# Kernel tuning notes

Hardware: AMD Instinct MI355X
Metric: run time of the kernel (lower is better)

The kernel has to match this reference:

```python
import math
import jax, jax.numpy as jnp
import numpy as np

B, L, D = 32, 512, 768
PAD, SEP = 0, 102
NEG = -9e15


def setup_inputs() -> dict:
    key = jax.random.key(0)
    ks = jax.random.split(key, 24)
    x = jax.random.normal(ks[0], (B, L, D), jnp.float32)
    # token ids: real tokens in [103, 30000), one SEP mid-sequence, PAD tail
    tok = jax.random.randint(ks[1], (B, L), 103, 30000)
    valid_len = jax.random.randint(ks[2], (B,), L // 2, L + 1)
    sep_pos = valid_len // 2
    pos = jnp.arange(L)[None, :]
    x_ids = jnp.where(pos < valid_len[:, None], tok, PAD)
    x_ids = jnp.where(pos == sep_pos[:, None], SEP, x_ids)

    s = 0.02
    def w(k, shape):
        return jax.random.normal(k, shape, jnp.float32) * s

    inp = dict(x=x, x_ids=x_ids, pad_idx=PAD, sep_idx=SEP)
    inp['W_anom'] = w(ks[3], (D, 1)); inp['b_anom'] = jnp.zeros((1,), jnp.float32)
    names = ['Wq_sup', 'Wk_sup', 'Wq_con', 'Wk_con', 'Wq_rep', 'Wk_rep']
    for i, n in enumerate(names):
        inp[n] = w(ks[4 + i], (D, D))
        inp[n.replace('W', 'b')] = jnp.zeros((D,), jnp.float32)
    inp['W_fuse1'] = w(ks[10], (3 * D, D)); inp['b_fuse1'] = jnp.zeros((D,), jnp.float32)
    inp['W_fuse2'] = w(ks[11], (D, D)); inp['b_fuse2'] = jnp.zeros((D,), jnp.float32)
    inp['ln_g'] = jnp.ones((D,), jnp.float32); inp['ln_b'] = jnp.zeros((D,), jnp.float32)
    return inp


def _segment_masks(x_ids, pad_idx, sep_idx, L):
    sep_mask = x_ids == sep_idx
    has_sep = sep_mask.any(axis=1)
    idxs = jnp.argmax(sep_mask.astype(jnp.int32), axis=1)
    valid_mask = x_ids != pad_idx
    valid_len = valid_mask.sum(axis=1)
    fallback = jnp.clip(valid_len // 2, 1, max(1, L - 2))
    sep_pos = jnp.where(has_sep, idxs, fallback)
    pos = jnp.arange(L)[None, :]
    false_mask = (pos < sep_pos[:, None]) & valid_mask
    option_mask = (pos > sep_pos[:, None]) & valid_mask
    return false_mask, option_mask


def reference(x, x_ids, pad_idx, sep_idx,
              W_anom, b_anom,
              Wq_sup, bq_sup, Wk_sup, bk_sup,
              Wq_con, bq_con, Wk_con, bk_con,
              Wq_rep, bq_rep, Wk_rep, bk_rep,
              W_fuse1, b_fuse1, W_fuse2, b_fuse2,
              ln_g, ln_b):
    Bx, Lx, Dm = x.shape
    false_mask, option_mask = _segment_masks(x_ids, pad_idx, sep_idx, Lx)

    # anomaly gate over the false (pre-SEP) segment
    anom = (x @ W_anom)[..., 0] + b_anom[0]                      # [B,L]
    anom = jnp.where(false_mask, anom, NEG)
    gate = jax.nn.softmax(anom, axis=1) * false_mask
    gate = gate / jnp.clip(gate.sum(axis=1, keepdims=True), 1e-8)

    inv = 1.0 / math.sqrt(Dm)
    q_sup = x @ Wq_sup + bq_sup; k_sup = x @ Wk_sup + bk_sup
    q_con = x @ Wq_con + bq_con; k_con = x @ Wk_con + bk_con
    q_rep = x @ Wq_rep + bq_rep; k_rep = x @ Wk_rep + bk_rep

    sup_scores = jnp.einsum('bld,bmd->blm', q_sup, k_sup) * inv   # [B,L,L]
    con_scores = jnp.einsum('bld,bmd->blm', q_con, k_con) * inv
    rep_scores = jnp.einsum('bld,bmd->blm', q_rep, k_rep) * inv

    pair_mask = false_mask[:, :, None] & option_mask[:, None, :]  # [B,L,L]
    sup_attn = jax.nn.softmax(jnp.where(pair_mask, sup_scores, NEG), axis=-1)
    conflict_signed = jnp.tanh(con_scores)
    rep_attn = jax.nn.softmax(jnp.where(pair_mask, rep_scores + conflict_signed, NEG), axis=-1)

    repair_token_vec = jnp.einsum('blm,bmd->bld', rep_attn, x)
    support_token_vec = jnp.einsum('blm,bmd->bld', sup_attn, x)

    anomaly_false_vec = jnp.einsum('bl,bld->bd', gate, x)
    weighted_repair_vec = jnp.einsum('bl,bld->bd', gate, repair_token_vec)
    weighted_support_vec = jnp.einsum('bl,bld->bd', gate, support_token_vec)

    fused = jnp.concatenate([anomaly_false_vec, weighted_repair_vec, weighted_support_vec], axis=-1)
    fused = jax.nn.relu(fused @ W_fuse1 + b_fuse1) @ W_fuse2 + b_fuse2  # dropout = identity (eval)

    mu = fused.mean(axis=-1, keepdims=True)
    var = ((fused - mu) ** 2).mean(axis=-1, keepdims=True)
    fused = (fused - mu) / jnp.sqrt(var + 1e-5) * ln_g + ln_b
    return fused
```

## Files before the change

kernel.cpp:

```cpp
#include <hip/hip_runtime.h>
#include <hip/hip_bf16.h>

#define B_ 32
#define L_ 512
#define D_ 768
#define M_ (B_*L_)
#define NEGV (-9e15f)

typedef __hip_bfloat16 bf16;
typedef short v8s __attribute__((ext_vector_type(8)));
typedef float v4f __attribute__((ext_vector_type(4)));

static __device__ __forceinline__ unsigned short f2b(float f) {
    __hip_bfloat16 h = __float2bfloat16(f);
    return *reinterpret_cast<unsigned short*>(&h);
}

static __device__ __forceinline__ float fast_tanh(float x) {
    x = fminf(fmaxf(x, -15.f), 15.f);
    float e2 = __expf(2.f * x);
    return (e2 - 1.f) / (e2 + 1.f);
}

static __device__ __forceinline__ void gl_lds16(const void* g, void* l) {
    __builtin_amdgcn_global_load_lds(
        (const __attribute__((address_space(1))) unsigned int*)g,
        (__attribute__((address_space(3))) unsigned int*)l, 16, 0, 0);
}

static __device__ __forceinline__ v8s pack8(const float* p) {
    v8s r;
    #pragma unroll
    for (int i = 0; i < 8; i++) r[i] = (short)f2b(p[i]);
    return r;
}

__global__ __launch_bounds__(256) void k_setup(const int* ids, const int* pad_p, const int* sep_p, int* seg,
                        const float* Wk_sup, const float* bq_sup,
                        const float* Wk_con, const float* bq_con,
                        const float* Wk_rep, const float* bq_rep,
                        const float* Wq_con, const float* bk_con,
                        float* __restrict__ vecs) {
    int bid = blockIdx.x, t = threadIdx.x;
    if (bid < 32) {
        int b = bid;
        __shared__ int red[256];
        int pad = *pad_p, sepid = *sep_p;
        int minsep = L_, vcount = 0;
        for (int l = t; l < L_; l += 256) {
            int id = ids[b*L_ + l];
            if (id == sepid && l < minsep) minsep = l;
            if (id != pad) vcount++;
        }
        red[t] = minsep; __syncthreads();
        for (int s = 128; s > 0; s >>= 1) { if (t < s) red[t] = min(red[t], red[t+s]); __syncthreads(); }
        int sepmin = red[0]; __syncthreads();
        red[t] = vcount; __syncthreads();
        for (int s = 128; s > 0; s >>= 1) { if (t < s) red[t] += red[t+s]; __syncthreads(); }
        if (t == 0) {
            int vlen = red[0];
            int fb = vlen / 2; if (fb < 1) fb = 1; if (fb > L_-2) fb = L_-2;
            int sep = (sepmin < L_) ? sepmin : fb;
            seg[b*2] = sep; seg[b*2+1] = vlen;
        }
        return;
    }
    {
        int gw = (bid - 32)*4 + (t >> 6);
        int lane = t & 63;
        if (gw > 3072) return;
        if (gw == 3072) {
            float s = 0.f;
            #pragma unroll
            for (int i = 0; i < D_/64; i++) s += bq_con[lane + 64*i] * bk_con[lane + 64*i];
            #pragma unroll
            for (int m = 32; m; m >>= 1) s += __shfl_xor(s, m);
            if (lane == 0) vecs[3072] = s;
            return;
        }
        int sel = gw / D_, row = gw % D_;
        const float* Wrow; const float* bv;
        switch (sel) {
            case 0: Wrow = Wk_sup + (size_t)row*D_; bv = bq_sup; break;
            case 1: Wrow = Wk_con + (size_t)row*D_; bv = bq_con; break;
            case 2: Wrow = Wk_rep + (size_t)row*D_; bv = bq_rep; break;
            default: Wrow = Wq_con + (size_t)row*D_; bv = bk_con; break;
        }
        float s = 0.f;
        #pragma unroll
        for (int i = 0; i < D_/64; i++) s += Wrow[lane + 64*i] * bv[lane + 64*i];
        #pragma unroll
        for (int m = 32; m; m >>= 1) s += __shfl_xor(s, m);
        if (lane == 0) vecs[gw] = s;
    }
}

__global__ void k_prep(const float* __restrict__ x, const float* __restrict__ Wa,
                       const float* __restrict__ ba, const float* __restrict__ vecs,
                       bf16* __restrict__ xb,
                       float* __restrict__ anom, float* __restrict__ csup,
                       float* __restrict__ ccon, float* __restrict__ crep,
                       float* __restrict__ rcon) {
    int gw = (blockIdx.x*blockDim.x + threadIdx.x) >> 6;
    int lane = threadIdx.x & 63;
    if (gw >= M_) return;
    const float* xr = x + (size_t)gw*D_;
    bf16* xbr = xb + (size_t)gw*D_;
    float sa=0.f, s0=0.f, s1=0.f, s2=0.f, s3=0.f;
    #pragma unroll
    for (int i = 0; i < D_/64; i++) {
        int o = i*64 + lane;
        float xv = xr[o];
        xbr[o] = __float2bfloat16(xv);
        sa += xv * Wa[o];
        s0 += xv * vecs[o];
        s1 += xv * vecs[768 + o];
        s2 += xv * vecs[1536 + o];
        s3 += xv * vecs[2304 + o];
    }
    #pragma unroll
    for (int m = 32; m; m >>= 1) {
        sa += __shfl_xor(sa, m); s0 += __shfl_xor(s0, m); s1 += __shfl_xor(s1, m);
        s2 += __shfl_xor(s2, m); s3 += __shfl_xor(s3, m);
    }
    if (lane == 0) {
        anom[gw] = sa + ba[0];
        csup[gw] = s0; ccon[gw] = s1; crep[gw] = s2; rcon[gw] = s3;
    }
}

__global__ void k_gate(const float* __restrict__ anom, const int* __restrict__ ids,
                       const int* seg, const int* pad_p, float* __restrict__ gate,
                       float4* __restrict__ zbuf, int zcount4) {
    int b = blockIdx.x, t = threadIdx.x;
    for (int i = b*256 + t; i < zcount4; i += 32*256)
        zbuf[i] = (float4){0.f,0.f,0.f,0.f};
    int sep = seg[b*2]; int pad = *pad_p;
    __shared__ float red[256];
    float a0[2]; bool f0[2];
    float mx = -__builtin_inff();
    #pragma unroll
    for (int j = 0; j < 2; j++) {
        int l = t + j*256;
        bool fm = (l < sep) && (ids[b*L_+l] != pad);
        float a = anom[b*L_+l];
        f0[j] = fm; a0[j] = a;
        if (fm) mx = fmaxf(mx, a);
    }
    red[t] = mx; __syncthreads();
    for (int s = 128; s; s >>= 1) { if (t < s) red[t] = fmaxf(red[t], red[t+s]); __syncthreads(); }
    mx = red[0]; __syncthreads();
    float e[2]; float se = 0.f;
    #pragma unroll
    for (int j = 0; j < 2; j++) { e[j] = f0[j] ? __expf(a0[j]-mx) : 0.f; se += e[j]; }
    red[t] = se; __syncthreads();
    for (int s = 128; s; s >>= 1) { if (t < s) red[t] += red[t+s]; __syncthreads(); }
    se = red[0];
    float inv = 1.f / fmaxf(se, 1e-8f);
    #pragma unroll
    for (int j = 0; j < 2; j++) { int l = t + j*256; gate[b*L_+l] = e[j]*inv; }
}

__global__ __launch_bounds__(256) void k_wqk(const float* Wq_sup, const float* Wk_sup,
                                             const float* Wq_con, const float* Wk_con,
                                             const float* Wq_rep, const float* Wk_rep,
                                             bf16* __restrict__ AT) {
    int h = blockIdx.z;
    const float* Asrc; const float* Bsrc;
    switch (h) { case 0: Asrc=Wk_sup; Bsrc=Wq_sup; break;
                 case 1: Asrc=Wk_con; Bsrc=Wq_con; break;
                 default: Asrc=Wk_rep; Bsrc=Wq_rep; }
    bf16* outp = AT + (size_t)h*D_*D_;
    __shared__ bf16 As[64*32];
    __shared__ bf16 Bs[64*32];
    int t = threadIdx.x;
    int wave = t >> 6, lane = t & 63;
    int quad = lane >> 4, l16 = lane & 15;
    int wm = wave >> 1, wn = wave & 1;
    int row0 = blockIdx.x * 64;
    int col0 = blockIdx.y * 64;

    v4f acc[2][2];
    #pragma unroll
    for (int i = 0; i < 2; i++)
        #pragma unroll
        for (int j = 0; j < 2; j++) acc[i][j] = (v4f){0.f,0.f,0.f,0.f};

    int srow = lane >> 2;
    int sk8  = lane & 3;
    int slot = (sk8 << 4) | srow;
    for (int k0 = 0; k0 < D_; k0 += 32) {
        #pragma unroll
        for (int cc = 0; cc < 2; cc++) {
            int c = wave + cc*4;
            const float* src = (c < 4)
                ? Asrc + (size_t)(row0 + c*16 + srow)*D_ + k0 + sk8*8
                : Bsrc + (size_t)(col0 + (c-4)*16 + srow)*D_ + k0 + sk8*8;
            float tmp[8];
            *reinterpret_cast<float4*>(tmp)     = *reinterpret_cast<const float4*>(src);
            *reinterpret_cast<float4*>(tmp + 4) = *reinterpret_cast<const float4*>(src + 4);
            v8s packed = pack8(tmp);
            if (c < 4) *reinterpret_cast<v8s*>(&As[(c    )*512 + slot*8]) = packed;
            else       *reinterpret_cast<v8s*>(&Bs[(c - 4)*512 + slot*8]) = packed;
        }
        __syncthreads();
        v8s af[2], bf[2];
        #pragma unroll
        for (int i = 0; i < 2; i++)
            af[i] = *reinterpret_cast<const v8s*>(&As[(wm*2 + i)*512 + lane*8]);
        #pragma unroll
        for (int j = 0; j < 2; j++)
            bf[j] = *reinterpret_cast<const v8s*>(&Bs[(wn*2 + j)*512 + lane*8]);
        #pragma unroll
        for (int i = 0; i < 2; i++)
            #pragma unroll
            for (int j = 0; j < 2; j++)
                acc[i][j] = __builtin_amdgcn_mfma_f32_16x16x32_bf16(af[i], bf[j], acc[i][j], 0, 0, 0);
        __syncthreads();
    }
    #pragma unroll
    for (int i = 0; i < 2; i++)
        #pragma unroll
        for (int j = 0; j < 2; j++) {
            int n = col0 + wn*32 + j*16 + l16;
            #pragma unroll
            for (int r = 0; r < 4; r++) {
                int m = row0 + wm*32 + i*16 + quad*4 + r;
                outp[(size_t)m*D_ + n] = __float2bfloat16(acc[i][j][r]);
            }
        }
}

__global__ __launch_bounds__(256) void k_gmat(const bf16* __restrict__ xb,
                                              const bf16* __restrict__ AT,
                                              const int* __restrict__ seg,
                                              bf16* __restrict__ G) {
    int b = blockIdx.x;
    int mt = blockIdx.y / 6, nt = blockIdx.y % 6;
    int h = blockIdx.z;
    int sep = seg[b*2];
    int row0 = mt*128;
    if (row0 >= sep) return;
    const bf16* Asrc = xb + (size_t)b*L_*D_;
    const bf16* Bsrc = AT + (size_t)h*D_*D_;
    bf16* outp = G + (size_t)(h*B_ + b)*L_*D_;
    __shared__ bf16 As[128*32];
    __shared__ bf16 Bs[128*32];
    int t = threadIdx.x;
    int wave = t >> 6, lane = t & 63;
    int quad = lane >> 4, l16 = lane & 15;
    int wm = wave >> 1, wn = wave & 1;
    int col0 = nt * 128;

    v4f acc[4][4];
    #pragma unroll
    for (int i = 0; i < 4; i++)
        #pragma unroll
        for (int j = 0; j < 4; j++) acc[i][j] = (v4f){0.f,0.f,0.f,0.f};

    int srow = lane >> 2;
    int skx  = ((lane & 3) ^ (srow & 3)) * 8;
    const bf16* agp0 = Asrc + (size_t)(row0 + wave*32 + srow)*D_ + skx;
    const bf16* agp1 = agp0 + 16*D_;
    const bf16* bgp0 = Bsrc + (size_t)(col0 + wave*32 + srow)*D_ + skx;
    const bf16* bgp1 = bgp0 + 16*D_;
    bf16* al0 = &As[(wave*2    )*512];
    bf16* al1 = &As[(wave*2 + 1)*512];
    bf16* bl0 = &Bs[(wave*2    )*512];
    bf16* bl1 = &Bs[(wave*2 + 1)*512];
    int aoffA[4], aoffB[4];
    #pragma unroll
    for (int i = 0; i < 4; i++) {
        aoffA[i] = (wm*4 + i)*512 + (l16*4 + (quad ^ (l16 & 3)))*8;
        aoffB[i] = (wn*4 + i)*512 + (l16*4 + (quad ^ (l16 & 3)))*8;
    }

    for (int k0 = 0; k0 < D_; k0 += 32) {
        gl_lds16(agp0 + k0, al0);
        gl_lds16(agp1 + k0, al1);
        gl_lds16(bgp0 + k0, bl0);
        gl_lds16(bgp1 + k0, bl1);
        __syncthreads();
        v8s af[4], bf[4];
        #pragma unroll
        for (int i = 0; i < 4; i++)
            af[i] = *reinterpret_cast<const v8s*>(&As[aoffA[i]]);
        #pragma unroll
        for (int j = 0; j < 4; j++)
            bf[j] = *reinterpret_cast<const v8s*>(&Bs[aoffB[j]]);
        #pragma unroll
        for (int i = 0; i < 4; i++)
            #pragma unroll
            for (int j = 0; j < 4; j++)
                acc[i][j] = __builtin_amdgcn_mfma_f32_16x16x32_bf16(af[i], bf[j], acc[i][j], 0, 0, 0);
        __syncthreads();
    }
    #pragma unroll
    for (int i = 0; i < 4; i++)
        #pragma unroll
        for (int j = 0; j < 4; j++) {
            int n = col0 + wn*64 + j*16 + l16;
            #pragma unroll
            for (int r = 0; r < 4; r++) {
                int m = row0 + wm*64 + i*16 + quad*4 + r;
                outp[(size_t)m*D_ + n] = __float2bfloat16(acc[i][j][r]);
            }
        }
}

__global__ __launch_bounds__(256) void k_score(const bf16* __restrict__ G,
                                               const bf16* __restrict__ xb,
                                               const int* __restrict__ ids,
                                               const int* __restrict__ seg,
                                               const float* __restrict__ gate,
                                               const int* pad_p,
                                               const float* __restrict__ csup,
                                               const float* __restrict__ ccon,
                                               const float* __restrict__ crep,
                                               const float* __restrict__ rcon,
                                               const float* __restrict__ vecs,
                                               float* __restrict__ w_sup,
                                               float* __restrict__ w_rep) {
    int b = blockIdx.x, rt = blockIdx.y;
    int sep = seg[b*2];
    int r0 = rt*16;
    if (r0 >= sep) return;
    int pad = *pad_p;
    int wave = threadIdx.x >> 6, lane = threadIdx.x & 63;
    int quad = lane >> 4, l16 = lane & 15;
    const float inv  = 0.03608439182435161f;
    int ct0 = (sep + 1) >> 4;

    __shared__ bf16 Gs[3*12288];
    {
        int srow = lane >> 2;
        int sk8  = lane & 3;
        int slot = (sk8 << 4) | srow;
        for (int c = wave; c < 72; c += 4) {
            int h = c / 24, kb = c % 24;
            const bf16* gsrc = G + (size_t)(h*B_ + b)*L_*D_ + (size_t)(r0 + srow)*D_ + kb*32 + sk8*8;
            v8s v = *reinterpret_cast<const v8s*>(gsrc);
            *reinterpret_cast<v8s*>(&Gs[h*12288 + kb*512 + slot*8]) = v;
        }
    }

    int tile[6]; bool act[6];
    #pragma unroll
    for (int i = 0; i < 6; i++) {
        int ctv = ct0 + wave + 4*i;
        act[i] = ctv < 32;
        tile[i] = act[i] ? ctv : 31;
    }
    int koff[6];
    #pragma unroll
    for (int i = 0; i < 6; i++) koff[i] = (tile[i]*16 + l16)*D_ + quad*8;

    v4f S[6], C[6], R[6];
    #pragma unroll
    for (int i = 0; i < 6; i++) { S[i] = (v4f){0,0,0,0}; C[i] = (v4f){0,0,0,0}; R[i] = (v4f){0,0,0,0}; }

    const bf16* xrow = xb + (size_t)b*L_*D_;

    __syncthreads();
    for (int k0 = 0, kb = 0; k0 < D_; k0 += 32, kb++) {
        v8s as = *reinterpret_cast<const v8s*>(&Gs[          kb*512 + lane*8]);
        v8s ac = *reinterpret_cast<const v8s*>(&Gs[12288 + kb*512 + lane*8]);
        v8s ar = *reinterpret_cast<const v8s*>(&Gs[24576 + kb*512 + lane*8]);
        #pragma unroll
        for (int i = 0; i < 6; i++) {
            v8s kf = *reinterpret_cast<const v8s*>(xrow + koff[i] + k0);
            S[i] = __builtin_amdgcn_mfma_f32_16x16x32_bf16(as, kf, S[i], 0, 0, 0);
            C[i] = __builtin_amdgcn_mfma_f32_16x16x32_bf16(ac, kf, C[i], 0, 0, 0);
            R[i] = __builtin_amdgcn_mfma_f32_16x16x32_bf16(ar, kf, R[i], 0, 0, 0);
        }
    }

    bool opt[6];
    float cs_v[6], cc_v[6], cr_v[6];
    #pragma unroll
    for (int i = 0; i < 6; i++) {
        int c = tile[i]*16 + l16;
        opt[i] = act[i] && (c > sep) && (ids[b*L_ + c] != pad);
        cs_v[i] = csup[b*L_ + c];
        cc_v[i] = ccon[b*L_ + c];
        cr_v[i] = crep[b*L_ + c];
    }
    float rc_r[4];
    #pragma unroll
    for (int r = 0; r < 4; r++) rc_r[r] = rcon[b*L_ + r0 + quad*4 + r];
    float dcon = vecs[3072];

    #pragma unroll
    for (int i = 0; i < 6; i++)
        #pragma unroll
        for (int r = 0; r < 4; r++) {
            float sl = (S[i][r] + cs_v[i]) * inv;
            float cl = fast_tanh((C[i][r] + cc_v[i] + rc_r[r] + dcon) * inv);
            float rl = (R[i][r] + cr_v[i]) * inv + cl;
            S[i][r] = sl; R[i][r] = rl;
        }

    float mxs[4], mxr[4];
    #pragma unroll
    for (int r = 0; r < 4; r++) { mxs[r] = NEGV; mxr[r] = NEGV; }
    #pragma unroll
    for (int i = 0; i < 6; i++)
        #pragma unroll
        for (int r = 0; r < 4; r++) {
            float sv = opt[i] ? S[i][r] : NEGV;
            float rv = opt[i] ? R[i][r] : NEGV;
            mxs[r] = fmaxf(mxs[r], sv);
            mxr[r] = fmaxf(mxr[r], rv);
        }
    #pragma unroll
    for (int d = 1; d < 16; d <<= 1)
        #pragma unroll
        for (int r = 0; r < 4; r++) {
            mxs[r] = fmaxf(mxs[r], __shfl_xor(mxs[r], d));
            mxr[r] = fmaxf(mxr[r], __shfl_xor(mxr[r], d));
        }
    __shared__ float redm[2][16][4];
    __shared__ float reds[2][16][4];
    if (l16 == 0)
        #pragma unroll
        for (int r = 0; r < 4; r++) {
            redm[0][quad*4+r][wave] = mxs[r];
            redm[1][quad*4+r][wave] = mxr[r];
        }
    __syncthreads();
    #pragma unroll
    for (int r = 0; r < 4; r++) {
        int row = quad*4 + r;
        mxs[r] = fmaxf(fmaxf(redm[0][row][0], redm[0][row][1]), fmaxf(redm[0][row][2], redm[0][row][3]));
        mxr[r] = fmaxf(fmaxf(redm[1][row][0], redm[1][row][1]), fmaxf(redm[1][row][2], redm[1][row][3]));
    }

    float ssum[4] = {0,0,0,0}, rsum[4] = {0,0,0,0};
    #pragma unroll
    for (int i = 0; i < 6; i++)
        #pragma unroll
        for (int r = 0; r < 4; r++) {
            float es = opt[i] ? __expf(S[i][r] - mxs[r]) : 0.f;
            float er = opt[i] ? __expf(R[i][r] - mxr[r]) : 0.f;
            S[i][r] = es; R[i][r] = er;
            ssum[r] += es; rsum[r] += er;
        }
    #pragma unroll
    for (int d = 1; d < 16; d <<= 1)
        #pragma unroll
        for (int r = 0; r < 4; r++) {
            ssum[r] += __shfl_xor(ssum[r], d);
            rsum[r] += __shfl_xor(rsum[r], d);
        }
    if (l16 == 0)
        #pragma unroll
        for (int r = 0; r < 4; r++) {
            reds[0][quad*4+r][wave] = ssum[r];
            reds[1][quad*4+r][wave] = rsum[r];
        }
    __syncthreads();
    float gs_[4], gr_[4];
    #pragma unroll
    for (int r = 0; r < 4; r++) {
        int row = quad*4 + r;
        float st = reds[0][row][0] + reds[0][row][1] + reds[0][row][2] + reds[0][row][3];
        float rtot = reds[1][row][0] + reds[1][row][1] + reds[1][row][2] + reds[1][row][3];
        float g = gate[b*L_ + r0 + row];
        gs_[r] = g / st;
        gr_[r] = g / rtot;
    }

    #pragma unroll
    for (int i = 0; i < 6; i++) {
        float cs = 0.f, cr = 0.f;
        #pragma unroll
        for (int r = 0; r < 4; r++) { cs += S[i][r]*gs_[r]; cr += R[i][r]*gr_[r]; }
        cs += __shfl_xor(cs, 16); cs += __shfl_xor(cs, 32);
        cr += __shfl_xor(cr, 16); cr += __shfl_xor(cr, 32);
        if (act[i] && quad == 0) {
            int c = tile[i]*16 + l16;
            atomicAdd(&w_sup[b*L_ + c], cs);
            atomicAdd(&w_rep[b*L_ + c], cr);
        }
    }
}

__global__ __launch_bounds__(256) void k_fused(const bf16* __restrict__ xb,
                                               const float* __restrict__ gate,
                                               const float* __restrict__ wrep,
                                               const float* __restrict__ wsup,
                                               float* __restrict__ fused) {
    int b = blockIdx.x, ch = blockIdx.y, t = threadIdx.x;
    int l0 = ch*64;
    const bf16* xb_ = xb + (size_t)b*L_*D_;
    float a0=0,a1=0,a2=0, r0=0,r1=0,r2=0, s0=0,s1=0,s2=0;
    for (int l = l0; l < l0+64; l++) {
        float g = gate[b*L_+l], wr = wrep[b*L_+l], wv = wsup[b*L_+l];
        if (g == 0.f && wr == 0.f && wv == 0.f) continue;
        float x0 = __bfloat162float(xb_[l*D_ + t]);
        float x1 = __bfloat162float(xb_[l*D_ + t + 256]);
        float x2 = __bfloat162float(xb_[l*D_ + t + 512]);
        a0 += g*x0;  a1 += g*x1;  a2 += g*x2;
        r0 += wr*x0; r1 += wr*x1; r2 += wr*x2;
        s0 += wv*x0; s1 += wv*x1; s2 += wv*x2;
    }
    float* f = fused + (size_t)b*2304;
    atomicAdd(&f[t],        a0); atomicAdd(&f[t+256],      a1); atomicAdd(&f[t+512],      a2);
    atomicAdd(&f[768+t],    r0); atomicAdd(&f[768+t+256],  r1); atomicAdd(&f[768+t+512],  r2);
    atomicAdd(&f[1536+t],   s0); atomicAdd(&f[1536+t+256], s1); atomicAdd(&f[1536+t+512], s2);
}

__global__ __launch_bounds__(256) void k_mlp1(const float* __restrict__ fused,
                                              const float* __restrict__ W1,
                                              float* __restrict__ h1pre) {
    int c0 = blockIdx.x*64, k0 = blockIdx.y*128;
    int t = threadIdx.x;
    __shared__ float fsl[32][132];
    for (int i = t*4; i < 32*128; i += 1024) {
        int b = i >> 7, k = i & 127;
        const float4 v = *reinterpret_cast<const float4*>(&fused[(size_t)b*2304 + k0 + k]);
        fsl[b][k] = v.x; fsl[b][k+1] = v.y; fsl[b][k+2] = v.z; fsl[b][k+3] = v.w;
    }
    __syncthreads();
    int c = c0 + (t & 63), bg = (t >> 6) * 8;
    float acc[8] = {0,0,0,0,0,0,0,0};
    for (int k = 0; k < 128; k++) {
        float w = W1[(size_t)(k0+k)*D_ + c];
        #pragma unroll
        for (int b = 0; b < 8; b++) acc[b] += fsl[bg+b][k] * w;
    }
    #pragma unroll
    for (int b = 0; b < 8; b++) atomicAdd(&h1pre[(size_t)(bg+b)*D_ + c], acc[b]);
}

__global__ __launch_bounds__(256) void k_mlp2(const float* __restrict__ h1pre,
                                              const float* __restrict__ b1,
                                              const float* __restrict__ W2,
                                              float* __restrict__ opre) {
    int c0 = blockIdx.x*64, k0 = blockIdx.y*128;
    int t = threadIdx.x;
    __shared__ float fsl[32][132];
    for (int i = t*4; i < 32*128; i += 1024) {
        int b = i >> 7, k = i & 127;
        const float4 v = *reinterpret_cast<const float4*>(&h1pre[(size_t)b*D_ + k0 + k]);
        const float4 bb = *reinterpret_cast<const float4*>(&b1[k0 + k]);
        fsl[b][k]   = fmaxf(v.x + bb.x, 0.f);
        fsl[b][k+1] = fmaxf(v.y + bb.y, 0.f);
        fsl[b][k+2] = fmaxf(v.z + bb.z, 0.f);
        fsl[b][k+3] = fmaxf(v.w + bb.w, 0.f);
    }
    __syncthreads();
    int c = c0 + (t & 63), bg = (t >> 6) * 8;
    float acc[8] = {0,0,0,0,0,0,0,0};
    for (int k = 0; k < 128; k++) {
        float w = W2[(size_t)(k0+k)*D_ + c];
        #pragma unroll
        for (int b = 0; b < 8; b++) acc[b] += fsl[bg+b][k] * w;
    }
    #pragma unroll
    for (int b = 0; b < 8; b++) atomicAdd(&opre[(size_t)(bg+b)*D_ + c], acc[b]);
}

__global__ __launch_bounds__(256) void k_ln(const float* __restrict__ opre,
                                            const float* __restrict__ b2,
                                            const float* __restrict__ lng,
                                            const float* __restrict__ lnb,
                                            float* __restrict__ out) {
    int b = blockIdx.x, t = threadIdx.x;
    __shared__ float red[256];
    float v0 = opre[(size_t)b*D_ + t]       + b2[t];
    float v1 = opre[(size_t)b*D_ + t + 256] + b2[t+256];
    float v2 = opre[(size_t)b*D_ + t + 512] + b2[t+512];
    float sum = v0+v1+v2, sq = v0*v0+v1*v1+v2*v2;
    red[t] = sum; __syncthreads();
    for (int s = 128; s; s >>= 1) { if (t < s) red[t] += red[t+s]; __syncthreads(); }
    sum = red[0]; __syncthreads();
    red[t] = sq; __syncthreads();
    for (int s = 128; s; s >>= 1) { if (t < s) red[t] += red[t+s]; __syncthreads(); }
    sq = red[0];
    float mu = sum / 768.f;
    float var = sq / 768.f - mu*mu;
    float rstd = rsqrtf(var + 1e-5f);
    out[(size_t)b*D_ + t]       = (v0-mu)*rstd*lng[t]     + lnb[t];
    out[(size_t)b*D_ + t + 256] = (v1-mu)*rstd*lng[t+256] + lnb[t+256];
    out[(size_t)b*D_ + t + 512] = (v2-mu)*rstd*lng[t+512] + lnb[t+512];
}

extern "C" void kernel_launch(void* const* d_in, const int* in_sizes, int n_in,
                              void* d_out, int out_size, void* d_ws, size_t ws_size,
                              hipStream_t stream) {
    const float* x      = (const float*)d_in[0];
    const int*   ids    = (const int*)d_in[1];
    const int*   pad_p  = (const int*)d_in[2];
    const int*   sep_p  = (const int*)d_in[3];
    const float* W_anom = (const float*)d_in[4];
    const float* b_anom = (const float*)d_in[5];
    const float* Wq_sup = (const float*)d_in[6];  const float* bq_sup = (const float*)d_in[7];
    const float* Wk_sup = (const float*)d_in[8];  const float* bk_sup = (const float*)d_in[9];
    const float* Wq_con = (const float*)d_in[10]; const float* bq_con = (const float*)d_in[11];
    const float* Wk_con = (const float*)d_in[12]; const float* bk_con = (const float*)d_in[13];
    const float* Wq_rep = (const float*)d_in[14]; const float* bq_rep = (const float*)d_in[15];
    const float* Wk_rep = (const float*)d_in[16]; const float* bk_rep = (const float*)d_in[17];
    const float* W1     = (const float*)d_in[18]; const float* b1     = (const float*)d_in[19];
    const float* W2     = (const float*)d_in[20]; const float* b2     = (const float*)d_in[21];
    const float* lng    = (const float*)d_in[22]; const float* lnb    = (const float*)d_in[23];
    float* out = (float*)d_out;

    char* w = (char*)d_ws;
    bf16*  xb    = (bf16*)(w);
    bf16*  AT    = (bf16*)(w + 25165824);
    bf16*  G     = (bf16*)(w + 28704768);
    float* vecs  = (float*)(w + 104202240);
    float* anom  = (float*)(w + 104218624);
    float* gate  = (float*)(w + 104284160);
    float* csup  = (float*)(w + 104349696);
    float* ccon  = (float*)(w + 104415232);
    float* crep  = (float*)(w + 104480768);
    float* rcon  = (float*)(w + 104546304);
    float* wsup  = (float*)(w + 104611840);
    float* wrep  = (float*)(w + 104677376);
    float* fused = (float*)(w + 104742912);
    float* h1pre = (float*)(w + 105037824);
    float* opre  = (float*)(w + 105136128);
    int*   seg   = (int*)  (w + 105234432);

    k_setup<<<801, 256, 0, stream>>>(ids, pad_p, sep_p, seg,
                                     Wk_sup, bq_sup, Wk_con, bq_con, Wk_rep, bq_rep, Wq_con, bk_con, vecs);
    k_prep<<<4096, 256, 0, stream>>>(x, W_anom, b_anom, vecs, xb, anom, csup, ccon, crep, rcon);
    k_gate<<<B_, 256, 0, stream>>>(anom, ids, seg, pad_p, gate, (float4*)wsup, 38912);
    k_wqk<<<dim3(12, 12, 3), 256, 0, stream>>>(Wq_sup, Wk_sup, Wq_con, Wk_con, Wq_rep, Wk_rep, AT);
    k_gmat<<<dim3(B_, 12, 3), 256, 0, stream>>>(xb, AT, seg, G);
    k_score<<<dim3(B_, 16), 256, 0, stream>>>(G, xb, ids, seg, gate, pad_p,
                                              csup, ccon, crep, rcon, vecs, wsup, wrep);
    k_fused<<<dim3(B_, 8), 256, 0, stream>>>(xb, gate, wrep, wsup, fused);
    k_mlp1<<<dim3(12, 18), 256, 0, stream>>>(fused, W1, h1pre);
    k_mlp2<<<dim3(12, 6), 256, 0, stream>>>(h1pre, b1, W2, opre);
    k_ln<<<B_, 256, 0, stream>>>(opre, b2, lng, lnb, out);
}
```

Before: 339.1 us.

## Fuse G-matrix projection into score kernel, dropping the global G buffer

After: 661.3 us. +95.0%, slower.

```diff
diff --git a/kernel.cpp b/kernel.cpp
--- a/kernel.cpp
+++ b/kernel.cpp
@@ -20,12 +20,6 @@
     x = fminf(fmaxf(x, -15.f), 15.f);
     float e2 = __expf(2.f * x);
     return (e2 - 1.f) / (e2 + 1.f);
-}
-
-static __device__ __forceinline__ void gl_lds16(const void* g, void* l) {
-    __builtin_amdgcn_global_load_lds(
-        (const __attribute__((address_space(1))) unsigned int*)g,
-        (__attribute__((address_space(3))) unsigned int*)l, 16, 0, 0);
 }
 
 static __device__ __forceinline__ v8s pack8(const float* p) {
@@ -231,96 +225,19 @@
         }
 }
 
-__global__ __launch_bounds__(256) void k_gmat(const bf16* __restrict__ xb,
-                                              const bf16* __restrict__ AT,
-                                              const int* __restrict__ seg,
-                                              bf16* __restrict__ G) {
-    int b = blockIdx.x;
-    int mt = blockIdx.y / 6, nt = blockIdx.y % 6;
-    int h = blockIdx.z;
-    int sep = seg[b*2];
-    int row0 = mt*128;
-    if (row0 >= sep) return;
-    const bf16* Asrc = xb + (size_t)b*L_*D_;
-    const bf16* Bsrc = AT + (size_t)h*D_*D_;
-    bf16* outp = G + (size_t)(h*B_ + b)*L_*D_;
-    __shared__ bf16 As[128*32];
-    __shared__ bf16 Bs[128*32];
-    int t = threadIdx.x;
-    int wave = t >> 6, lane = t & 63;
-    int quad = lane >> 4, l16 = lane & 15;
-    int wm = wave >> 1, wn = wave & 1;
-    int col0 = nt * 128;
-
-    v4f acc[4][4];
-    #pragma unroll
-    for (int i = 0; i < 4; i++)
-        #pragma unroll
-        for (int j = 0; j < 4; j++) acc[i][j] = (v4f){0.f,0.f,0.f,0.f};
-
-    int srow = lane >> 2;
-    int skx  = ((lane & 3) ^ (srow & 3)) * 8;
-    const bf16* agp0 = Asrc + (size_t)(row0 + wave*32 + srow)*D_ + skx;
-    const bf16* agp1 = agp0 + 16*D_;
-    const bf16* bgp0 = Bsrc + (size_t)(col0 + wave*32 + srow)*D_ + skx;
-    const bf16* bgp1 = bgp0 + 16*D_;
-    bf16* al0 = &As[(wave*2    )*512];
-    bf16* al1 = &As[(wave*2 + 1)*512];
-    bf16* bl0 = &Bs[(wave*2    )*512];
-    bf16* bl1 = &Bs[(wave*2 + 1)*512];
-    int aoffA[4], aoffB[4];
-    #pragma unroll
-    for (int i = 0; i < 4; i++) {
-        aoffA[i] = (wm*4 + i)*512 + (l16*4 + (quad ^ (l16 & 3)))*8;
-        aoffB[i] = (wn*4 + i)*512 + (l16*4 + (quad ^ (l16 & 3)))*8;
-    }
-
-    for (int k0 = 0; k0 < D_; k0 += 32) {
-        gl_lds16(agp0 + k0, al0);
-        gl_lds16(agp1 + k0, al1);
-        gl_lds16(bgp0 + k0, bl0);
-        gl_lds16(bgp1 + k0, bl1);
-        __syncthreads();
-        v8s af[4], bf[4];
-        #pragma unroll
-        for (int i = 0; i < 4; i++)
-            af[i] = *reinterpret_cast<const v8s*>(&As[aoffA[i]]);
-        #pragma unroll
-        for (int j = 0; j < 4; j++)
-            bf[j] = *reinterpret_cast<const v8s*>(&Bs[aoffB[j]]);
-        #pragma unroll
-        for (int i = 0; i < 4; i++)
-            #pragma unroll
-            for (int j = 0; j < 4; j++)
-                acc[i][j] = __builtin_amdgcn_mfma_f32_16x16x32_bf16(af[i], bf[j], acc[i][j], 0, 0, 0);
-        __syncthreads();
-    }
-    #pragma unroll
-    for (int i = 0; i < 4; i++)
-        #pragma unroll
-        for (int j = 0; j < 4; j++) {
-            int n = col0 + wn*64 + j*16 + l16;
-            #pragma unroll
-            for (int r = 0; r < 4; r++) {
-                int m = row0 + wm*64 + i*16 + quad*4 + r;
-                outp[(size_t)m*D_ + n] = __float2bfloat16(acc[i][j][r]);
-            }
-        }
-}
-
-__global__ __launch_bounds__(256) void k_score(const bf16* __restrict__ G,
-                                               const bf16* __restrict__ xb,
-                                               const int* __restrict__ ids,
-                                               const int* __restrict__ seg,
-                                               const float* __restrict__ gate,
-                                               const int* pad_p,
-                                               const float* __restrict__ csup,
-                                               const float* __restrict__ ccon,
-                                               const float* __restrict__ crep,
-                                               const float* __restrict__ rcon,
-                                               const float* __restrict__ vecs,
-                                               float* __restrict__ w_sup,
-                                               float* __restrict__ w_rep) {
+__global__ __launch_bounds__(256) void k_gscore(const bf16* __restrict__ xb,
+                                                const bf16* __restrict__ AT,
+                                                const int* __restrict__ ids,
+                                                const int* __restrict__ seg,
+                                                const float* __restrict__ gate,
+                                                const int* pad_p,
+                                                const float* __restrict__ csup,
+                                                const float* __restrict__ ccon,
+                                                const float* __restrict__ crep,
+                                                const float* __restrict__ rcon,
+                                                const float* __restrict__ vecs,
+                                                float* __restrict__ w_sup,
+                                                float* __restrict__ w_rep) {
     int b = blockIdx.x, rt = blockIdx.y;
     int sep = seg[b*2];
     int r0 = rt*16;
@@ -328,19 +245,21 @@
     int pad = *pad_p;
     int wave = threadIdx.x >> 6, lane = threadIdx.x & 63;
     int quad = lane >> 4, l16 = lane & 15;
-    const float inv  = 0.03608439182435161f;
+    int lane8 = lane*8;
+    const float inv = 0.03608439182435161f;
     int ct0 = (sep + 1) >> 4;
 
-    __shared__ bf16 Gs[3*12288];
+    __shared__ bf16 Xs[12288];
+    __shared__ bf16 Gs[12288];
+
+    const bf16* xrow = xb + (size_t)b*L_*D_;
+
     {
-        int srow = lane >> 2;
-        int sk8  = lane & 3;
+        int srow = lane >> 2, sk8 = lane & 3;
         int slot = (sk8 << 4) | srow;
-        for (int c = wave; c < 72; c += 4) {
-            int h = c / 24, kb = c % 24;
-            const bf16* gsrc = G + (size_t)(h*B_ + b)*L_*D_ + (size_t)(r0 + srow)*D_ + kb*32 + sk8*8;
-            v8s v = *reinterpret_cast<const v8s*>(gsrc);
-            *reinterpret_cast<v8s*>(&Gs[h*12288 + kb*512 + slot*8]) = v;
+        for (int kb = wave; kb < 24; kb += 4) {
+            v8s v = *reinterpret_cast<const v8s*>(xrow + (size_t)(r0 + srow)*D_ + kb*32 + sk8*8);
+            *reinterpret_cast<v8s*>(&Xs[kb*512 + slot*8]) = v;
         }
     }
 
@@ -355,23 +274,69 @@
     #pragma unroll
     for (int i = 0; i < 6; i++) koff[i] = (tile[i]*16 + l16)*D_ + quad*8;
 
+    int voff[12];
+    #pragma unroll
+    for (int gi = 0; gi < 12; gi++)
+        voff[gi] = ((wave + 4*gi)*16 + l16)*D_ + quad*8;
+
     v4f S[6], C[6], R[6];
     #pragma unroll
     for (int i = 0; i < 6; i++) { S[i] = (v4f){0,0,0,0}; C[i] = (v4f){0,0,0,0}; R[i] = (v4f){0,0,0,0}; }
 
-    const bf16* xrow = xb + (size_t)b*L_*D_;
-
     __syncthreads();
-    for (int k0 = 0, kb = 0; k0 < D_; k0 += 32, kb++) {
-        v8s as = *reinterpret_cast<const v8s*>(&Gs[          kb*512 + lane*8]);
-        v8s ac = *reinterpret_cast<const v8s*>(&Gs[12288 + kb*512 + lane*8]);
-        v8s ar = *reinterpret_cast<const v8s*>(&Gs[24576 + kb*512 + lane*8]);
-        #pragma unroll
-        for (int i = 0; i < 6; i++) {
-            v8s kf = *reinterpret_cast<const v8s*>(xrow + koff[i] + k0);
-            S[i] = __builtin_amdgcn_mfma_f32_16x16x32_bf16(as, kf, S[i], 0, 0, 0);
-            C[i] = __builtin_amdgcn_mfma_f32_16x16x32_bf16(ac, kf, C[i], 0, 0, 0);
-            R[i] = __builtin_amdgcn_mfma_f32_16x16x32_bf16(ar, kf, R[i], 0, 0, 0);
+
+    #pragma unroll
+    for (int h = 0; h < 3; h++) {
+        const bf16* ATh = AT + (size_t)h*D_*D_;
+        v4f gacc[12];
+        #pragma unroll
+        for (int gi = 0; gi < 12; gi++) gacc[gi] = (v4f){0,0,0,0};
+        for (int kb = 0; kb < 24; kb++) {
+            v8s xa = *reinterpret_cast<const v8s*>(&Xs[kb*512 + lane8]);
+            #pragma unroll
+            for (int gi = 0; gi < 12; gi++) {
+                v8s bt = *reinterpret_cast<const v8s*>(ATh + voff[gi] + kb*32);
+                gacc[gi] = __builtin_amdgcn_mfma_f32_16x16x32_bf16(xa, bt, gacc[gi], 0, 0, 0);
+            }
+        }
+        if (h > 0) __syncthreads();
+        #pragma unroll
+        for (int gi = 0; gi < 12; gi++) {
+            int v = (wave + 4*gi)*16 + l16;
+            int kb = v >> 5, q8 = (v >> 3) & 3, j = v & 7;
+            int base = kb*512 + q8*128 + j;
+            #pragma unroll
+            for (int r = 0; r < 4; r++)
+                Gs[base + (quad*4 + r)*8] = __float2bfloat16(gacc[gi][r]);
+        }
+        __syncthreads();
+        if (h == 0) {
+            for (int kb = 0, k0 = 0; kb < 24; kb++, k0 += 32) {
+                v8s ga = *reinterpret_cast<const v8s*>(&Gs[kb*512 + lane8]);
+                #pragma unroll
+                for (int i = 0; i < 6; i++) {
+                    v8s kf = *reinterpret_cast<const v8s*>(xrow + koff[i] + k0);
+                    S[i] = __builtin_amdgcn_mfma_f32_16x16x32_bf16(ga, kf, S[i], 0, 0, 0);
+                }
+            }
+        } else if (h == 1) {
+            for (int kb = 0, k0 = 0; kb < 24; kb++, k0 += 32) {
+                v8s ga = *reinterpret_cast<const v8s*>(&Gs[kb*512 + lane8]);
+                #pragma unroll
+                for (int i = 0; i < 6; i++) {
+                    v8s kf = *reinterpret_cast<const v8s*>(xrow + koff[i] + k0);
+                    C[i] = __builtin_amdgcn_mfma_f32_16x16x32_bf16(ga, kf, C[i], 0, 0, 0);
+                }
+            }
+        } else {
+            for (int kb = 0, k0 = 0; kb < 24; kb++, k0 += 32) {
+                v8s ga = *reinterpret_cast<const v8s*>(&Gs[kb*512 + lane8]);
+                #pragma unroll
+                for (int i = 0; i < 6; i++) {
+                    v8s kf = *reinterpret_cast<const v8s*>(xrow + koff[i] + k0);
+                    R[i] = __builtin_amdgcn_mfma_f32_16x16x32_bf16(ga, kf, R[i], 0, 0, 0);
+                }
+            }
         }
     }
 
@@ -609,29 +574,27 @@
     char* w = (char*)d_ws;
     bf16*  xb    = (bf16*)(w);
     bf16*  AT    = (bf16*)(w + 25165824);
-    bf16*  G     = (bf16*)(w + 28704768);
-    float* vecs  = (float*)(w + 104202240);
-    float* anom  = (float*)(w + 104218624);
-    float* gate  = (float*)(w + 104284160);
-    float* csup  = (float*)(w + 104349696);
-    float* ccon  = (float*)(w + 104415232);
-    float* crep  = (float*)(w + 104480768);
-    float* rcon  = (float*)(w + 104546304);
-    float* wsup  = (float*)(w + 104611840);
-    float* wrep  = (float*)(w + 104677376);
-    float* fused = (float*)(w + 104742912);
-    float* h1pre = (float*)(w + 105037824);
-    float* opre  = (float*)(w + 105136128);
-    int*   seg   = (int*)  (w + 105234432);
+    float* vecs  = (float*)(w + 28704768);
+    float* anom  = (float*)(w + 28721152);
+    float* gate  = (float*)(w + 28786688);
+    float* csup  = (float*)(w + 28852224);
+    float* ccon  = (float*)(w + 28917760);
+    float* crep  = (float*)(w + 28983296);
+    float* rcon  = (float*)(w + 29048832);
+    float* wsup  = (float*)(w + 29114368);
+    float* wrep  = (float*)(w + 29179904);
+    float* fused = (float*)(w + 29245440);
+    float* h1pre = (float*)(w + 29540352);
+    float* opre  = (float*)(w + 29638656);
+    int*   seg   = (int*)  (w + 29736960);
 
     k_setup<<<801, 256, 0, stream>>>(ids, pad_p, sep_p, seg,
                                      Wk_sup, bq_sup, Wk_con, bq_con, Wk_rep, bq_rep, Wq_con, bk_con, vecs);
     k_prep<<<4096, 256, 0, stream>>>(x, W_anom, b_anom, vecs, xb, anom, csup, ccon, crep, rcon);
     k_gate<<<B_, 256, 0, stream>>>(anom, ids, seg, pad_p, gate, (float4*)wsup, 38912);
     k_wqk<<<dim3(12, 12, 3), 256, 0, stream>>>(Wq_sup, Wk_sup, Wq_con, Wk_con, Wq_rep, Wk_rep, AT);
-    k_gmat<<<dim3(B_, 12, 3), 256, 0, stream>>>(xb, AT, seg, G);
-    k_score<<<dim3(B_, 16), 256, 0, stream>>>(G, xb, ids, seg, gate, pad_p,
-                                              csup, ccon, crep, rcon, vecs, wsup, wrep);
+    k_gscore<<<dim3(B_, 16), 256, 0, stream>>>(xb, AT, ids, seg, gate, pad_p,
+                                               csup, ccon, crep, rcon, vecs, wsup, wrep);
     k_fused<<<dim3(B_, 8), 256, 0, stream>>>(xb, gate, wrep, wsup, fused);
     k_mlp1<<<dim3(12, 18), 256, 0, stream>>>(fused, W1, h1pre);
     k_mlp2<<<dim3(12, 6), 256, 0, stream>>>(h1pre, b1, W2, opre);
```

## Merge prep and weight-product kernels; drop max-subtraction in score softmax

Applied to the files above, without the earlier changes.

New measurement: 336.7 us. About the same (-0.7%).

```diff
diff --git a/kernel.cpp b/kernel.cpp
--- a/kernel.cpp
+++ b/kernel.cpp
@@ -95,90 +95,61 @@
     }
 }
 
-__global__ void k_prep(const float* __restrict__ x, const float* __restrict__ Wa,
+__global__ __launch_bounds__(256) void k_prepw(const float* __restrict__ x, const float* __restrict__ Wa,
                        const float* __restrict__ ba, const float* __restrict__ vecs,
                        bf16* __restrict__ xb,
                        float* __restrict__ anom, float* __restrict__ csup,
                        float* __restrict__ ccon, float* __restrict__ crep,
-                       float* __restrict__ rcon) {
-    int gw = (blockIdx.x*blockDim.x + threadIdx.x) >> 6;
-    int lane = threadIdx.x & 63;
-    if (gw >= M_) return;
-    const float* xr = x + (size_t)gw*D_;
-    bf16* xbr = xb + (size_t)gw*D_;
-    float sa=0.f, s0=0.f, s1=0.f, s2=0.f, s3=0.f;
-    #pragma unroll
-    for (int i = 0; i < D_/64; i++) {
-        int o = i*64 + lane;
-        float xv = xr[o];
-        xbr[o] = __float2bfloat16(xv);
-        sa += xv * Wa[o];
-        s0 += xv * vecs[o];
-        s1 += xv * vecs[768 + o];
-        s2 += xv * vecs[1536 + o];
-        s3 += xv * vecs[2304 + o];
-    }
-    #pragma unroll
-    for (int m = 32; m; m >>= 1) {
-        sa += __shfl_xor(sa, m); s0 += __shfl_xor(s0, m); s1 += __shfl_xor(s1, m);
-        s2 += __shfl_xor(s2, m); s3 += __shfl_xor(s3, m);
-    }
-    if (lane == 0) {
-        anom[gw] = sa + ba[0];
-        csup[gw] = s0; ccon[gw] = s1; crep[gw] = s2; rcon[gw] = s3;
-    }
-}
-
-__global__ void k_gate(const float* __restrict__ anom, const int* __restrict__ ids,
-                       const int* seg, const int* pad_p, float* __restrict__ gate,
-                       float4* __restrict__ zbuf, int zcount4) {
-    int b = blockIdx.x, t = threadIdx.x;
-    for (int i = b*256 + t; i < zcount4; i += 32*256)
-        zbuf[i] = (float4){0.f,0.f,0.f,0.f};
-    int sep = seg[b*2]; int pad = *pad_p;
-    __shared__ float red[256];
-    float a0[2]; bool f0[2];
-    float mx = -__builtin_inff();
-    #pragma unroll
-    for (int j = 0; j < 2; j++) {
-        int l = t + j*256;
-        bool fm = (l < sep) && (ids[b*L_+l] != pad);
-        float a = anom[b*L_+l];
-        f0[j] = fm; a0[j] = a;
-        if (fm) mx = fmaxf(mx, a);
-    }
-    red[t] = mx; __syncthreads();
-    for (int s = 128; s; s >>= 1) { if (t < s) red[t] = fmaxf(red[t], red[t+s]); __syncthreads(); }
-    mx = red[0]; __syncthreads();
-    float e[2]; float se = 0.f;
-    #pragma unroll
-    for (int j = 0; j < 2; j++) { e[j] = f0[j] ? __expf(a0[j]-mx) : 0.f; se += e[j]; }
-    red[t] = se; __syncthreads();
-    for (int s = 128; s; s >>= 1) { if (t < s) red[t] += red[t+s]; __syncthreads(); }
-    se = red[0];
-    float inv = 1.f / fmaxf(se, 1e-8f);
-    #pragma unroll
-    for (int j = 0; j < 2; j++) { int l = t + j*256; gate[b*L_+l] = e[j]*inv; }
-}
-
-__global__ __launch_bounds__(256) void k_wqk(const float* Wq_sup, const float* Wk_sup,
-                                             const float* Wq_con, const float* Wk_con,
-                                             const float* Wq_rep, const float* Wk_rep,
-                                             bf16* __restrict__ AT) {
-    int h = blockIdx.z;
+                       float* __restrict__ rcon,
+                       const float* Wq_sup, const float* Wk_sup,
+                       const float* Wq_con, const float* Wk_con,
+                       const float* Wq_rep, const float* Wk_rep,
+                       bf16* __restrict__ AT) {
+    __shared__ bf16 As[64*32];
+    __shared__ bf16 Bs[64*32];
+    int bid = blockIdx.x;
+    if (bid < 4096) {
+        int gw = (bid*256 + threadIdx.x) >> 6;
+        int lane = threadIdx.x & 63;
+        const float* xr = x + (size_t)gw*D_;
+        bf16* xbr = xb + (size_t)gw*D_;
+        float sa=0.f, s0=0.f, s1=0.f, s2=0.f, s3=0.f;
+        #pragma unroll
+        for (int i = 0; i < D_/64; i++) {
+            int o = i*64 + lane;
+            float xv = xr[o];
+            xbr[o] = __float2bfloat16(xv);
+            sa += xv * Wa[o];
+            s0 += xv * vecs[o];
+            s1 += xv * vecs[768 + o];
+            s2 += xv * vecs[1536 + o];
+            s3 += xv * vecs[2304 + o];
+        }
+        #pragma unroll
+        for (int m = 32; m; m >>= 1) {
+            sa += __shfl_xor(sa, m); s0 += __shfl_xor(s0, m); s1 += __shfl_xor(s1, m);
+            s2 += __shfl_xor(s2, m); s3 += __shfl_xor(s3, m);
+        }
+        if (lane == 0) {
+            anom[gw] = sa + ba[0];
+            csup[gw] = s0; ccon[gw] = s1; crep[gw] = s2; rcon[gw] = s3;
+        }
+        return;
+    }
+    int wid = bid - 4096;
+    int h = wid / 144, rem = wid % 144;
+    int bx = rem / 12, by = rem % 12;
     const float* Asrc; const float* Bsrc;
     switch (h) { case 0: Asrc=Wk_sup; Bsrc=Wq_sup; break;
                  case 1: Asrc=Wk_con; Bsrc=Wq_con; break;
                  default: Asrc=Wk_rep; Bsrc=Wq_rep; }
     bf16* outp = AT + (size_t)h*D_*D_;
-    __shared__ bf16 As[64*32];
-    __shared__ bf16 Bs[64*32];
     int t = threadIdx.x;
     int wave = t >> 6, lane = t & 63;
     int quad = lane >> 4, l16 = lane & 15;
     int wm = wave >> 1, wn = wave & 1;
-    int row0 = blockIdx.x * 64;
-    int col0 = blockIdx.y * 64;
+    int row0 = bx * 64;
+    int col0 = by * 64;
 
     v4f acc[2][2];
     #pragma unroll
@@ -229,6 +200,38 @@
                 outp[(size_t)m*D_ + n] = __float2bfloat16(acc[i][j][r]);
             }
         }
+}
+
+__global__ void k_gate(const float* __restrict__ anom, const int* __restrict__ ids,
+                       const int* seg, const int* pad_p, float* __restrict__ gate,
+                       float4* __restrict__ zbuf, int zcount4) {
+    int b = blockIdx.x, t = threadIdx.x;
+    for (int i = b*256 + t; i < zcount4; i += 32*256)
+        zbuf[i] = (float4){0.f,0.f,0.f,0.f};
+    int sep = seg[b*2]; int pad = *pad_p;
+    __shared__ float red[256];
+    float a0[2]; bool f0[2];
+    float mx = -__builtin_inff();
+    #pragma unroll
+    for (int j = 0; j < 2; j++) {
+        int l = t + j*256;
+        bool fm = (l < sep) && (ids[b*L_+l] != pad);
+        float a = anom[b*L_+l];
+        f0[j] = fm; a0[j] = a;
+        if (fm) mx = fmaxf(mx, a);
+    }
+    red[t] = mx; __syncthreads();
+    for (int s = 128; s; s >>= 1) { if (t < s) red[t] = fmaxf(red[t], red[t+s]); __syncthreads(); }
+    mx = red[0]; __syncthreads();
+    float e[2]; float se = 0.f;
+    #pragma unroll
+    for (int j = 0; j < 2; j++) { e[j] = f0[j] ? __expf(a0[j]-mx) : 0.f; se += e[j]; }
+    red[t] = se; __syncthreads();
+    for (int s = 128; s; s >>= 1) { if (t < s) red[t] += red[t+s]; __syncthreads(); }
+    se = red[0];
+    float inv = 1.f / fmaxf(se, 1e-8f);
+    #pragma unroll
+    for (int j = 0; j < 2; j++) { int l = t + j*256; gate[b*L_+l] = e[j]*inv; }
 }
 
 __global__ __launch_bounds__(256) void k_gmat(const bf16* __restrict__ xb,
@@ -390,6 +393,7 @@
     for (int r = 0; r < 4; r++) rc_r[r] = rcon[b*L_ + r0 + quad*4 + r];
     float dcon = vecs[3072];
 
+    float ssum[4] = {0,0,0,0}, rsum[4] = {0,0,0,0};
     #pragma unroll
     for (int i = 0; i < 6; i++)
         #pragma unroll
@@ -397,51 +401,8 @@
             float sl = (S[i][r] + cs_v[i]) * inv;
             float cl = fast_tanh((C[i][r] + cc_v[i] + rc_r[r] + dcon) * inv);
             float rl = (R[i][r] + cr_v[i]) * inv + cl;
-            S[i][r] = sl; R[i][r] = rl;
-        }
-
-    float mxs[4], mxr[4];
-    #pragma unroll
-    for (int r = 0; r < 4; r++) { mxs[r] = NEGV; mxr[r] = NEGV; }
-    #pragma unroll
-    for (int i = 0; i < 6; i++)
-        #pragma unroll
-        for (int r = 0; r < 4; r++) {
-            float sv = opt[i] ? S[i][r] : NEGV;
-            float rv = opt[i] ? R[i][r] : NEGV;
-            mxs[r] = fmaxf(mxs[r], sv);
-            mxr[r] = fmaxf(mxr[r], rv);
-        }
-    #pragma unroll
-    for (int d = 1; d < 16; d <<= 1)
-        #pragma unroll
-        for (int r = 0; r < 4; r++) {
-            mxs[r] = fmaxf(mxs[r], __shfl_xor(mxs[r], d));
-            mxr[r] = fmaxf(mxr[r], __shfl_xor(mxr[r], d));
-        }
-    __shared__ float redm[2][16][4];
-    __shared__ float reds[2][16][4];
-    if (l16 == 0)
-        #pragma unroll
-        for (int r = 0; r < 4; r++) {
-            redm[0][quad*4+r][wave] = mxs[r];
-            redm[1][quad*4+r][wave] = mxr[r];
-        }
-    __syncthreads();
-    #pragma unroll
-    for (int r = 0; r < 4; r++) {
-        int row = quad*4 + r;
-        mxs[r] = fmaxf(fmaxf(redm[0][row][0], redm[0][row][1]), fmaxf(redm[0][row][2], redm[0][row][3]));
-        mxr[r] = fmaxf(fmaxf(redm[1][row][0], redm[1][row][1]), fmaxf(redm[1][row][2], redm[1][row][3]));
-    }
-
-    float ssum[4] = {0,0,0,0}, rsum[4] = {0,0,0,0};
-    #pragma unroll
-    for (int i = 0; i < 6; i++)
-        #pragma unroll
-        for (int r = 0; r < 4; r++) {
-            float es = opt[i] ? __expf(S[i][r] - mxs[r]) : 0.f;
-            float er = opt[i] ? __expf(R[i][r] - mxr[r]) : 0.f;
+            float es = opt[i] ? __expf(sl) : 0.f;
+            float er = opt[i] ? __expf(rl) : 0.f;
             S[i][r] = es; R[i][r] = er;
             ssum[r] += es; rsum[r] += er;
         }
@@ -452,6 +413,7 @@
             ssum[r] += __shfl_xor(ssum[r], d);
             rsum[r] += __shfl_xor(rsum[r], d);
         }
+    __shared__ float reds[2][16][4];
     if (l16 == 0)
         #pragma unroll
         for (int r = 0; r < 4; r++) {
@@ -626,9 +588,9 @@
 
     k_setup<<<801, 256, 0, stream>>>(ids, pad_p, sep_p, seg,
                                      Wk_sup, bq_sup, Wk_con, bq_con, Wk_rep, bq_rep, Wq_con, bk_con, vecs);
-    k_prep<<<4096, 256, 0, stream>>>(x, W_anom, b_anom, vecs, xb, anom, csup, ccon, crep, rcon);
+    k_prepw<<<4528, 256, 0, stream>>>(x, W_anom, b_anom, vecs, xb, anom, csup, ccon, crep, rcon,
+                                      Wq_sup, Wk_sup, Wq_con, Wk_con, Wq_rep, Wk_rep, AT);
     k_gate<<<B_, 256, 0, stream>>>(anom, ids, seg, pad_p, gate, (float4*)wsup, 38912);
-    k_wqk<<<dim3(12, 12, 3), 256, 0, stream>>>(Wq_sup, Wk_sup, Wq_con, Wk_con, Wq_rep, Wk_rep, AT);
     k_gmat<<<dim3(B_, 12, 3), 256, 0, stream>>>(xb, AT, seg, G);
     k_score<<<dim3(B_, 16), 256, 0, stream>>>(G, xb, ids, seg, gate, pad_p,
                                               csup, ccon, crep, rcon, vecs, wsup, wrep);
```
